# Optimization experiments

Hardware: AMD Instinct MI355X
Metric: run time of the kernel (lower is better)

## Reference

```python
import jax, jax.numpy as jnp
import numpy as np

B_, L_, D_, H_ = 2, 1024, 1024, 16


def _matrixR(L, d_model):
    # Transformer-XL sinusoid table, reversed along the position axis (reverse=True)
    inv_freq = 1.0 / (10000.0 ** (np.arange(0, d_model, 2, dtype=np.float32) / d_model))
    sinus = np.arange(L, dtype=np.float32)[:, None] * inv_freq[None, :]
    mat = np.zeros((L, d_model), dtype=np.float32)
    mat[:, 0::2] = np.sin(sinus)
    mat[:, 1::2] = np.cos(sinus)
    return jnp.asarray(mat[::-1].copy())


def _shift_b(x):
    # x: (b, h, L, L) -> TXL relative shift + lower-triangular mask
    b, h, L, _ = x.shape
    pad = jnp.concatenate([jnp.zeros((b, h, L, 1), x.dtype), x], axis=-1)  # (b,h,L,L+1)
    shifted = pad.reshape(b, h, L + 1, L)[:, :, 1:, :]                      # (b,h,L,L)
    return jnp.tril(shifted)


def setup_inputs() -> dict:
    key = jax.random.key(0)
    ks = jax.random.split(key, 8)
    s = 1.0 / np.sqrt(D_)
    return {
        "E": jax.random.normal(ks[0], (B_, L_, D_), dtype=jnp.float32),
        "Ev": jax.random.normal(ks[1], (B_, L_, D_), dtype=jnp.float32),
        "R": _matrixR(L_, D_),
        "Wq": jax.random.normal(ks[2], (D_, D_), dtype=jnp.float32) * s,
        "Wke": jax.random.normal(ks[3], (D_, D_), dtype=jnp.float32) * s,
        "Wkr": jax.random.normal(ks[4], (D_, D_), dtype=jnp.float32) * s,
        "Wv": jax.random.normal(ks[5], (D_, D_), dtype=jnp.float32) * s,
        "cb": jnp.ones((D_,), dtype=jnp.float32),
        "pb": jnp.ones((D_,), dtype=jnp.float32),
        "Wo_w": jax.random.normal(ks[6], (D_, D_), dtype=jnp.float32) * s,
        "Wo_b": jnp.zeros((D_,), dtype=jnp.float32),
        "ln_g": jnp.ones((D_,), dtype=jnp.float32),
        "ln_b": jnp.zeros((D_,), dtype=jnp.float32),
    }


def reference(E, Ev, R, Wq, Wke, Wkr, Wv, cb, pb, Wo_w, Wo_b, ln_g, ln_b):
    b, L, d = E.shape
    h = H_
    dh = d // h
    # projections -> (b, h, L, dh)
    q = (E @ Wq).reshape(b, L, h, dh).transpose(0, 2, 1, 3)
    k = (Ev @ Wke).reshape(b, L, h, dh).transpose(0, 2, 1, 3)
    v = (Ev @ Wv).reshape(b, L, h, dh).transpose(0, 2, 1, 3)
    # relative-position keys (batch independent): (h, L, dh)
    Q = (R @ Wkr).reshape(L, h, dh).transpose(1, 0, 2)
    # (a) content-content
    A_a = jnp.einsum('bhid,bhjd->bhij', q, k)
    # (b) content-position, with shift trick
    A_b = _shift_b(jnp.einsum('bhid,hjd->bhij', q, Q))
    # (c) global content bias (same for every query row)
    A_c = jnp.einsum('hd,bhjd->bhj', cb.reshape(h, dh), k)[:, :, None, :]  # (b,h,1,L)
    # (d) global position bias (batch independent), shifted
    d_row = jnp.einsum('hd,hjd->hj', pb.reshape(h, dh), Q)                 # (h,L)
    A_d = _shift_b(jnp.broadcast_to(d_row[None, :, None, :], (1, h, L, L)))
    A = A_a + A_b + A_c + A_d
    p = jax.nn.softmax(A, axis=-1)
    Oh = jnp.einsum('bhij,bhjd->bhid', p, v)
    O = Oh.transpose(0, 2, 1, 3).reshape(b, L, d)
    # residual + output proj (dropout is identity in eval) + LayerNorm
    res = Ev + (O @ Wo_w + Wo_b)
    mu = jnp.mean(res, axis=-1, keepdims=True)
    var = jnp.mean((res - mu) ** 2, axis=-1, keepdims=True)
    return (res - mu) * jax.lax.rsqrt(var + 1e-5) * ln_g + ln_b
```

## Files before the change

kernel.cpp:

```cpp
#include <hip/hip_runtime.h>
#include <hip/hip_bf16.h>
#include <math.h>

#define B_ 2
#define L_ 1024
#define D_ 1024
#define H_ 16

typedef short short8 __attribute__((ext_vector_type(8)));
typedef float f32x4  __attribute__((ext_vector_type(4)));

__device__ __forceinline__ short f2bf(float f) {
  unsigned u = __float_as_uint(f);
  u += 0x7fff + ((u >> 16) & 1);
  return (short)(u >> 16);
}
__device__ __forceinline__ float bf2f(short s) {
  return __uint_as_float(((unsigned)(unsigned short)s) << 16);
}
__device__ __forceinline__ int swz(int row, int slot) {
  return row * 64 + ((slot ^ (row & 7)) << 3);
}
__device__ __forceinline__ int vswz(int d, int j) {
  return d * 64 + ((((j >> 3) ^ (d & 7) ^ ((d >> 3) & 7)) & 7) << 3) + (j & 7);
}

__device__ __forceinline__ void glds16(const void* g, void* l) {
  __builtin_amdgcn_global_load_lds((const __attribute__((address_space(1))) void*)g,
                                   (__attribute__((address_space(3))) void*)l, 16, 0, 0);
}

__global__ __launch_bounds__(256) void castbf(
    const float* __restrict__ E, const float* __restrict__ Ev,
    const float* __restrict__ R, short* __restrict__ o) {
  size_t i8 = ((size_t)blockIdx.x * 256 + threadIdx.x) * 8;
  const float* src; size_t off;
  if (i8 < 2097152)      { src = E;  off = i8; }
  else if (i8 < 4194304) { src = Ev; off = i8 - 2097152; }
  else                   { src = R;  off = i8 - 4194304; }
  float4 a = *(const float4*)&src[off];
  float4 b = *(const float4*)&src[off + 4];
  short8 v;
  v[0] = f2bf(a.x); v[1] = f2bf(a.y); v[2] = f2bf(a.z); v[3] = f2bf(a.w);
  v[4] = f2bf(b.x); v[5] = f2bf(b.y); v[6] = f2bf(b.z); v[7] = f2bf(b.w);
  *(short8*)&o[i8] = v;
}

template<int OUT_F32>
__device__ __forceinline__ void mm_glds(const short* __restrict__ A,
                                        const short* __restrict__ Bt,
                                        void* Cp, int N, int K,
                                        int bx, int by) {
  __shared__ short As[8192];
  __shared__ short Bs[8192];
  const int tid = threadIdx.x;
  const int l = tid & 63, w = tid >> 6;
  const int row0 = by * 128, col0 = bx * 128;
  const int wm = (w >> 1) * 64, wn = (w & 1) * 64;
  const f32x4 fz = {0.f, 0.f, 0.f, 0.f};

  f32x4 acc[4][4];
  #pragma unroll
  for (int i = 0; i < 4; ++i)
    #pragma unroll
    for (int j = 0; j < 4; ++j) acc[i][j] = fz;

  const int lrow = l >> 3;
  const int lcol = (l & 7) * 8;

  for (int t = 0; t < K / 64; ++t) {
    const int k0 = t * 64;
    if (t) __syncthreads();
    #pragma unroll
    for (int c = 0; c < 4; ++c) {
      const int rr = (w * 4 + c) * 8 + lrow;
      glds16(&A[(size_t)(row0 + rr) * K + k0 + lcol], &As[(w * 4 + c) * 512]);
      glds16(&Bt[(size_t)(col0 + rr) * K + k0 + lcol], &Bs[(w * 4 + c) * 512]);
    }
    __syncthreads();
    #pragma unroll
    for (int kf = 0; kf < 2; ++kf) {
      short8 a[4], b[4];
      #pragma unroll
      for (int mf = 0; mf < 4; ++mf)
        a[mf] = *(const short8*)&As[(wm + mf * 16 + (l & 15)) * 64 + (kf * 4 + (l >> 4)) * 8];
      #pragma unroll
      for (int nf = 0; nf < 4; ++nf)
        b[nf] = *(const short8*)&Bs[(wn + nf * 16 + (l & 15)) * 64 + (kf * 4 + (l >> 4)) * 8];
      #pragma unroll
      for (int mf = 0; mf < 4; ++mf)
        #pragma unroll
        for (int nf = 0; nf < 4; ++nf)
          acc[mf][nf] = __builtin_amdgcn_mfma_f32_16x16x32_bf16(a[mf], b[nf], acc[mf][nf], 0, 0, 0);
    }
  }

  #pragma unroll
  for (int mf = 0; mf < 4; ++mf)
    #pragma unroll
    for (int nf = 0; nf < 4; ++nf)
      #pragma unroll
      for (int r = 0; r < 4; ++r) {
        int row = row0 + wm + mf * 16 + (l >> 4) * 4 + r;
        int col = col0 + wn + nf * 16 + (l & 15);
        if (OUT_F32) ((float*)Cp)[(size_t)row * N + col] = acc[mf][nf][r];
        else         ((short*)Cp)[(size_t)row * N + col] = f2bf(acc[mf][nf][r]);
      }
}

__global__ __launch_bounds__(256) void proj_mfma(
    const short* __restrict__ Eb, const short* __restrict__ Evb,
    const short* __restrict__ Rb, const short* __restrict__ Wt,
    short* __restrict__ qb, short* __restrict__ kb,
    short* __restrict__ vb, short* __restrict__ Qpb) {
  const int z = blockIdx.z;
  const short* A; const short* Bt; short* C; int M;
  const size_t MM = (size_t)D_ * D_;
  if (z == 0)      { A = Eb;  Bt = Wt;          C = qb;  M = B_ * L_; }
  else if (z == 1) { A = Evb; Bt = Wt + MM;     C = kb;  M = B_ * L_; }
  else if (z == 2) { A = Evb; Bt = Wt + 3 * MM; C = vb;  M = B_ * L_; }
  else             { A = Rb;  Bt = Wt + 2 * MM; C = Qpb; M = L_;      }
  if ((int)blockIdx.y * 128 >= M) return;
  mm_glds<0>(A, Bt, C, D_, D_, blockIdx.x, blockIdx.y);
}

__global__ __launch_bounds__(256) void out_mfma(
    const short* __restrict__ Ob, const short* __restrict__ Wot, float* __restrict__ proj) {
  mm_glds<1>(Ob, Wot, proj, D_, D_, blockIdx.x, blockIdx.y);
}

__global__ __launch_bounds__(256) void tcast(
    const float* __restrict__ W0, const float* __restrict__ W1,
    const float* __restrict__ W2, const float* __restrict__ W3,
    const float* __restrict__ W4, short* __restrict__ out) {
  const int z = blockIdx.z;
  const float* W = (z == 0) ? W0 : (z == 1) ? W1 : (z == 2) ? W2 : (z == 3) ? W3 : W4;
  short* Wt = out + (size_t)z * D_ * D_;
  __shared__ short t[64][65];
  const int tid = threadIdx.x;
  const int r0 = blockIdx.y * 64, c0 = blockIdx.x * 64;
  #pragma unroll
  for (int i = 0; i < 4; ++i) {
    int idx = tid + i * 256;
    int r = idx >> 4, c4 = (idx & 15) * 4;
    float4 v = *(const float4*)&W[(size_t)(r0 + r) * D_ + c0 + c4];
    t[c4 + 0][r] = f2bf(v.x); t[c4 + 1][r] = f2bf(v.y);
    t[c4 + 2][r] = f2bf(v.z); t[c4 + 3][r] = f2bf(v.w);
  }
  __syncthreads();
  #pragma unroll
  for (int i = 0; i < 2; ++i) {
    int idx = tid + i * 256;
    int rr = idx >> 3, cc = (idx & 7) * 8;
    short8 o;
    #pragma unroll
    for (int e = 0; e < 8; ++e) o[e] = t[rr][cc + e];
    *(short8*)&Wt[(size_t)(c0 + rr) * D_ + r0 + cc] = o;
  }
}

__global__ __launch_bounds__(256) void cdvec(
    const short* __restrict__ kb, const short* __restrict__ Qpb,
    const float* __restrict__ cb, const float* __restrict__ pb,
    float* __restrict__ cvec, float* __restrict__ dvec) {
  int idx = blockIdx.x * 256 + threadIdx.x;
  if (idx < B_ * H_ * L_) {
    int b = idx >> 14, h = (idx >> 10) & 15, j = idx & 1023;
    const short* kr = &kb[(size_t)(b * L_ + j) * D_ + h * 64];
    const float* cr = &cb[h * 64];
    float s = 0.f;
    #pragma unroll
    for (int d8 = 0; d8 < 8; ++d8) {
      short8 kv = *(const short8*)&kr[d8 * 8];
      #pragma unroll
      for (int e = 0; e < 8; ++e) s += bf2f(kv[e]) * cr[d8 * 8 + e];
    }
    cvec[idx] = s;
  } else {
    int i2 = idx - B_ * H_ * L_;
    if (i2 < H_ * L_) {
      int h = i2 >> 10, m = i2 & 1023;
      const short* qr = &Qpb[(size_t)m * D_ + h * 64];
      const float* pr = &pb[h * 64];
      float s = 0.f;
      #pragma unroll
      for (int d8 = 0; d8 < 8; ++d8) {
        short8 qv = *(const short8*)&qr[d8 * 8];
        #pragma unroll
        for (int e = 0; e < 8; ++e) s += bf2f(qv[e]) * pr[d8 * 8 + e];
      }
      dvec[i2] = s;
    }
  }
}

__global__ __launch_bounds__(256) void attn_mfma(
    const short* __restrict__ qb, const short* __restrict__ kb,
    const short* __restrict__ vb, const short* __restrict__ Qpb,
    const float* __restrict__ cvec, const float* __restrict__ dvec,
    short* __restrict__ Ob) {
  __shared__ short q_s[4096];
  __shared__ short k_s[4096];
  __shared__ short vt_s[4096];
  __shared__ short win_s[8192];
  __shared__ short pb_s[4 * 1312];
  __shared__ float cvec_s[64];
  __shared__ float dvec_s[128];

  const int tid = threadIdx.x;
  const int l = tid & 63, w = tid >> 6;
  const int nib = L_ / 64;
  const int b  = blockIdx.x / (H_ * nib);
  const int hh = (blockIdx.x / nib) % H_;
  const int i0 = (blockIdx.x % nib) * 64;
  const f32x4 fz = {0.f, 0.f, 0.f, 0.f};
  const short8 sz = {0, 0, 0, 0, 0, 0, 0, 0};

  short8 rk[2], rv[2], rw[4];
  float rc = 0.f, rd = 0.f;

  auto stage_load = [&](int jt) {
    const int j0 = jt * 64;
    const bool pos = (j0 <= i0);
    const int mbase = L_ - 64 - i0 + j0;
    #pragma unroll
    for (int c = 0; c < 2; ++c) {
      int ci = tid + c * 256;
      int r = ci >> 3, s = ci & 7;
      rk[c] = *(const short8*)&kb[(size_t)(b * L_ + j0 + r) * D_ + hh * 64 + s * 8];
      rv[c] = *(const short8*)&vb[(size_t)(b * L_ + j0 + r) * D_ + hh * 64 + s * 8];
    }
    if (pos) {
      #pragma unroll
      for (int c = 0; c < 4; ++c) {
        int ci = tid + c * 256;
        int mm = ci >> 3, s = ci & 7;
        int m = mbase + mm;
        rw[c] = (m < L_) ? *(const short8*)&Qpb[(size_t)m * D_ + hh * 64 + s * 8] : sz;
      }
      if (tid < 128) {
        int m = mbase + tid;
        rd = (m < L_) ? dvec[hh * L_ + m] : 0.f;
      }
    }
    if (tid < 64) rc = cvec[(size_t)(b * H_ + hh) * L_ + j0 + tid];
  };

  auto stage_write = [&](int jt) {
    const bool pos = (jt * 64 <= i0);
    #pragma unroll
    for (int c = 0; c < 2; ++c) {
      int ci = tid + c * 256;
      int r = ci >> 3, s = ci & 7;
      *(short8*)&k_s[swz(r, s)] = rk[c];
      #pragma unroll
      for (int e = 0; e < 8; ++e) {
        int d = s * 8 + e;
        vt_s[vswz(d, r)] = rv[c][e];
      }
    }
    if (pos) {
      #pragma unroll
      for (int c = 0; c < 4; ++c) {
        int ci = tid + c * 256;
        int mm = ci >> 3, s = ci & 7;
        *(short8*)&win_s[swz(mm, s)] = rw[c];
      }
      if (tid < 128) dvec_s[tid] = rd;
    }
    if (tid < 64) cvec_s[tid] = rc;
  };

  short8 rq[2];
  #pragma unroll
  for (int c = 0; c < 2; ++c) {
    int ci = tid + c * 256;
    int r = ci >> 3, s = ci & 7;
    rq[c] = *(const short8*)&qb[(size_t)(b * L_ + i0 + r) * D_ + hh * 64 + s * 8];
  }
  stage_load(0);
  #pragma unroll
  for (int c = 0; c < 2; ++c) {
    int ci = tid + c * 256;
    *(short8*)&q_s[swz(ci >> 3, ci & 7)] = rq[c];
  }
  __syncthreads();

  short8 aq[2];
  {
    int row = w * 16 + (l & 15);
    aq[0] = *(const short8*)&q_s[swz(row, (l >> 4))];
    aq[1] = *(const short8*)&q_s[swz(row, 4 + (l >> 4))];
  }

  float mrow[4], lrow[4];
  f32x4 oacc[4];
  #pragma unroll
  for (int r = 0; r < 4; ++r) { mrow[r] = -3.0e38f; lrow[r] = 0.f; }
  #pragma unroll
  for (int nf = 0; nf < 4; ++nf) oacc[nf] = fz;

  for (int jt = 0; jt < 16; ++jt) {
    const int j0 = jt * 64;
    const bool pos = (j0 <= i0);
    const bool diag = (j0 == i0);

    stage_write(jt);
    __syncthreads();
    if (jt < 15) stage_load(jt + 1);

    f32x4 sac[4];
    #pragma unroll
    for (int nf = 0; nf < 4; ++nf) sac[nf] = fz;
    #pragma unroll
    for (int kf = 0; kf < 2; ++kf) {
      #pragma unroll
      for (int nf = 0; nf < 4; ++nf) {
        short8 bk = *(const short8*)&k_s[swz(nf * 16 + (l & 15), kf * 4 + (l >> 4))];
        sac[nf] = __builtin_amdgcn_mfma_f32_16x16x32_bf16(aq[kf], bk, sac[nf], 0, 0, 0);
      }
    }

    if (pos) {
      f32x4 pacc[5];
      #pragma unroll
      for (int u = 0; u < 5; ++u) pacc[u] = fz;
      const int nf0 = 3 - w;
      #pragma unroll
      for (int kf = 0; kf < 2; ++kf) {
        #pragma unroll
        for (int u = 0; u < 5; ++u) {
          short8 bw = *(const short8*)&win_s[swz((nf0 + u) * 16 + (l & 15), kf * 4 + (l >> 4))];
          pacc[u] = __builtin_amdgcn_mfma_f32_16x16x32_bf16(aq[kf], bw, pacc[u], 0, 0, 0);
        }
      }
      const int pbb = w * 1312;
      #pragma unroll
      for (int u = 0; u < 5; ++u)
        #pragma unroll
        for (int r = 0; r < 4; ++r) {
          int row = (l >> 4) * 4 + r;
          pb_s[pbb + row * 82 + u * 16 + (l & 15)] = f2bf(pacc[u][r]);
        }
    }

    #pragma unroll
    for (int nf = 0; nf < 4; ++nf)
      #pragma unroll
      for (int r = 0; r < 4; ++r) {
        int rj = nf * 16 + (l & 15);
        float s = sac[nf][r] + cvec_s[rj];
        if (pos) {
          int ris = (l >> 4) * 4 + r;
          int rib = w * 16 + ris;
          if (!diag || rj <= rib) {
            s += bf2f(pb_s[w * 1312 + ris * 82 + (15 - ris + rj)]);
            s += dvec_s[63 - rib + rj];
          }
        }
        sac[nf][r] = s;
      }

    #pragma unroll
    for (int r = 0; r < 4; ++r) {
      float mx = fmaxf(fmaxf(sac[0][r], sac[1][r]), fmaxf(sac[2][r], sac[3][r]));
      #pragma unroll
      for (int off = 1; off < 16; off <<= 1)
        mx = fmaxf(mx, __shfl_xor(mx, off, 64));
      float mn = fmaxf(mrow[r], mx);
      float sc = __expf(mrow[r] - mn);
      mrow[r] = mn;
      float ls = 0.f;
      #pragma unroll
      for (int nf = 0; nf < 4; ++nf) {
        float p = __expf(sac[nf][r] - mn);
        sac[nf][r] = p;
        ls += p;
      }
      #pragma unroll
      for (int off = 1; off < 16; off <<= 1)
        ls += __shfl_xor(ls, off, 64);
      lrow[r] = lrow[r] * sc + ls;
      #pragma unroll
      for (int nf = 0; nf < 4; ++nf) oacc[nf][r] *= sc;
    }

    #pragma unroll
    for (int nf = 0; nf < 4; ++nf)
      #pragma unroll
      for (int r = 0; r < 4; ++r) {
        int row = (l >> 4) * 4 + r;
        int col = nf * 16 + (l & 15);
        pb_s[w * 1312 + row * 64 + (((col >> 3) ^ (row & 7)) << 3) + (col & 7)] = f2bf(sac[nf][r]);
      }

    #pragma unroll
    for (int kf = 0; kf < 2; ++kf) {
      int prow = l & 15;
      short8 ap = *(const short8*)&pb_s[w * 1312 + prow * 64 + (((kf * 4 + (l >> 4)) ^ (prow & 7)) << 3)];
      #pragma unroll
      for (int nf = 0; nf < 4; ++nf) {
        short8 bv = *(const short8*)&vt_s[vswz(nf * 16 + (l & 15), (kf * 4 + (l >> 4)) * 8)];
        oacc[nf] = __builtin_amdgcn_mfma_f32_16x16x32_bf16(ap, bv, oacc[nf], 0, 0, 0);
      }
    }
    __syncthreads();
  }

  #pragma unroll
  for (int r = 0; r < 4; ++r) {
    float inv = 1.f / lrow[r];
    #pragma unroll
    for (int nf = 0; nf < 4; ++nf) {
      int row = i0 + w * 16 + (l >> 4) * 4 + r;
      int col = hh * 64 + nf * 16 + (l & 15);
      Ob[(size_t)(b * L_ + row) * D_ + col] = f2bf(oacc[nf][r] * inv);
    }
  }
}

__global__ __launch_bounds__(256) void ln_kernel(
    const float* __restrict__ Ev, const float* __restrict__ proj,
    const float* __restrict__ Wo_b, const float* __restrict__ g,
    const float* __restrict__ beta, float* __restrict__ out) {
  const int row = blockIdx.x;
  __shared__ float red[8];
  const int tid = threadIdx.x;
  const int d = tid * 4;

  float4 e  = *(const float4*)&Ev[(size_t)row * D_ + d];
  float4 p  = *(const float4*)&proj[(size_t)row * D_ + d];
  float4 wb = *(const float4*)&Wo_b[d];
  float4 rr = { e.x + p.x + wb.x, e.y + p.y + wb.y,
                e.z + p.z + wb.z, e.w + p.w + wb.w };
  float sum = rr.x + rr.y + rr.z + rr.w;
  float sq  = rr.x * rr.x + rr.y * rr.y + rr.z * rr.z + rr.w * rr.w;

  #pragma unroll
  for (int off = 1; off < 64; off <<= 1) {
    sum += __shfl_xor(sum, off, 64);
    sq  += __shfl_xor(sq,  off, 64);
  }
  const int wid = tid >> 6;
  if ((tid & 63) == 0) { red[wid * 2] = sum; red[wid * 2 + 1] = sq; }
  __syncthreads();
  sum = red[0] + red[2] + red[4] + red[6];
  sq  = red[1] + red[3] + red[5] + red[7];

  const float mu   = sum * (1.f / (float)D_);
  const float var  = sq * (1.f / (float)D_) - mu * mu;
  const float rstd = rsqrtf(var + 1e-5f);

  float4 gg = *(const float4*)&g[d];
  float4 bb = *(const float4*)&beta[d];
  float4 o = { (rr.x - mu) * rstd * gg.x + bb.x,
               (rr.y - mu) * rstd * gg.y + bb.y,
               (rr.z - mu) * rstd * gg.z + bb.z,
               (rr.w - mu) * rstd * gg.w + bb.w };
  *(float4*)&out[(size_t)row * D_ + d] = o;
}

extern "C" void kernel_launch(void* const* d_in, const int* in_sizes, int n_in,
                              void* d_out, int out_size, void* d_ws, size_t ws_size,
                              hipStream_t stream) {
  const float* E    = (const float*)d_in[0];
  const float* Ev   = (const float*)d_in[1];
  const float* R    = (const float*)d_in[2];
  const float* Wq   = (const float*)d_in[3];
  const float* Wke  = (const float*)d_in[4];
  const float* Wkr  = (const float*)d_in[5];
  const float* Wv   = (const float*)d_in[6];
  const float* cb   = (const float*)d_in[7];
  const float* pb   = (const float*)d_in[8];
  const float* Wo_w = (const float*)d_in[9];
  const float* Wo_b = (const float*)d_in[10];
  const float* ln_g = (const float*)d_in[11];
  const float* ln_b = (const float*)d_in[12];
  float* out = (float*)d_out;

  short* ws   = (short*)d_ws;
  short* Eb   = ws;
  short* Evb  = ws + 2097152;
  short* Rb   = ws + 4194304;
  short* qb   = ws + 5242880;
  short* kb   = ws + 7340032;
  short* vb   = ws + 9437184;
  short* Qpb  = ws + 11534336;
  short* Wt   = ws + 12582912;
  short* Ob   = ws + 17825792;
  float* proj = (float*)Eb;
  float* cvec = (float*)Rb;
  float* dvec = cvec + 32768;

  castbf<<<2560, 256, 0, stream>>>(E, Ev, R, Eb);

  tcast<<<dim3(16, 16, 5), 256, 0, stream>>>(Wq, Wke, Wkr, Wv, Wo_w, Wt);

  proj_mfma<<<dim3(8, 16, 4), 256, 0, stream>>>(Eb, Evb, Rb, Wt, qb, kb, vb, Qpb);

  cdvec<<<192, 256, 0, stream>>>(kb, Qpb, cb, pb, cvec, dvec);

  attn_mfma<<<B_ * H_ * (L_ / 64), 256, 0, stream>>>(qb, kb, vb, Qpb, cvec, dvec, Ob);

  out_mfma<<<dim3(8, 16), 256, 0, stream>>>(Ob, Wt + 4 * (size_t)D_ * D_, proj);

  ln_kernel<<<B_ * L_, 256, 0, stream>>>(Ev, proj, Wo_b, ln_g, ln_b, out);
}
```

Baseline: 227.0 us.

## Rewrite pipeline with single-wave direct-load GEMMs, fused biases, transposed V

Replaces the LDS-tiled 128x128 GEMMs with single-wave 32x64 tiles that load operands straight from global memory, and merges the activation cast and weight transpose kernels into one launch. The cvec/dvec kernel is removed by folding the content and position biases into q before the score MFMAs. V is written transposed by the projection so the attention kernel can read it directly. Attention now runs one wave per 16-row tile with no shared-memory staging or block barriers, using setprio around the MFMA sections. This cuts kernel launches and synchronisation, but relies on cache hits instead of LDS reuse and issues more redundant global loads.

```diff
diff --git a/kernel.cpp b/kernel.cpp
--- a/kernel.cpp
+++ b/kernel.cpp
@@ -8,6 +8,7 @@
 #define H_ 16
 
 typedef short short8 __attribute__((ext_vector_type(8)));
+typedef short short4v __attribute__((ext_vector_type(4)));
 typedef float f32x4  __attribute__((ext_vector_type(4)));
 
 __device__ __forceinline__ short f2bf(float f) {
@@ -18,127 +19,40 @@
 __device__ __forceinline__ float bf2f(short s) {
   return __uint_as_float(((unsigned)(unsigned short)s) << 16);
 }
-__device__ __forceinline__ int swz(int row, int slot) {
-  return row * 64 + ((slot ^ (row & 7)) << 3);
-}
-__device__ __forceinline__ int vswz(int d, int j) {
-  return d * 64 + ((((j >> 3) ^ (d & 7) ^ ((d >> 3) & 7)) & 7) << 3) + (j & 7);
-}
-
-__device__ __forceinline__ void glds16(const void* g, void* l) {
-  __builtin_amdgcn_global_load_lds((const __attribute__((address_space(1))) void*)g,
-                                   (__attribute__((address_space(3))) void*)l, 16, 0, 0);
-}
-
-__global__ __launch_bounds__(256) void castbf(
+__device__ __forceinline__ int pkey(int row) {
+  return (row & 7) ^ ((row & 8) >> 2);
+}
+
+__global__ __launch_bounds__(256) void prep(
     const float* __restrict__ E, const float* __restrict__ Ev,
-    const float* __restrict__ R, short* __restrict__ o) {
-  size_t i8 = ((size_t)blockIdx.x * 256 + threadIdx.x) * 8;
-  const float* src; size_t off;
-  if (i8 < 2097152)      { src = E;  off = i8; }
-  else if (i8 < 4194304) { src = Ev; off = i8 - 2097152; }
-  else                   { src = R;  off = i8 - 4194304; }
-  float4 a = *(const float4*)&src[off];
-  float4 b = *(const float4*)&src[off + 4];
-  short8 v;
-  v[0] = f2bf(a.x); v[1] = f2bf(a.y); v[2] = f2bf(a.z); v[3] = f2bf(a.w);
-  v[4] = f2bf(b.x); v[5] = f2bf(b.y); v[6] = f2bf(b.z); v[7] = f2bf(b.w);
-  *(short8*)&o[i8] = v;
-}
-
-template<int OUT_F32>
-__device__ __forceinline__ void mm_glds(const short* __restrict__ A,
-                                        const short* __restrict__ Bt,
-                                        void* Cp, int N, int K,
-                                        int bx, int by) {
-  __shared__ short As[8192];
-  __shared__ short Bs[8192];
-  const int tid = threadIdx.x;
-  const int l = tid & 63, w = tid >> 6;
-  const int row0 = by * 128, col0 = bx * 128;
-  const int wm = (w >> 1) * 64, wn = (w & 1) * 64;
-  const f32x4 fz = {0.f, 0.f, 0.f, 0.f};
-
-  f32x4 acc[4][4];
-  #pragma unroll
-  for (int i = 0; i < 4; ++i)
-    #pragma unroll
-    for (int j = 0; j < 4; ++j) acc[i][j] = fz;
-
-  const int lrow = l >> 3;
-  const int lcol = (l & 7) * 8;
-
-  for (int t = 0; t < K / 64; ++t) {
-    const int k0 = t * 64;
-    if (t) __syncthreads();
-    #pragma unroll
-    for (int c = 0; c < 4; ++c) {
-      const int rr = (w * 4 + c) * 8 + lrow;
-      glds16(&A[(size_t)(row0 + rr) * K + k0 + lcol], &As[(w * 4 + c) * 512]);
-      glds16(&Bt[(size_t)(col0 + rr) * K + k0 + lcol], &Bs[(w * 4 + c) * 512]);
-    }
-    __syncthreads();
-    #pragma unroll
-    for (int kf = 0; kf < 2; ++kf) {
-      short8 a[4], b[4];
-      #pragma unroll
-      for (int mf = 0; mf < 4; ++mf)
-        a[mf] = *(const short8*)&As[(wm + mf * 16 + (l & 15)) * 64 + (kf * 4 + (l >> 4)) * 8];
-      #pragma unroll
-      for (int nf = 0; nf < 4; ++nf)
-        b[nf] = *(const short8*)&Bs[(wn + nf * 16 + (l & 15)) * 64 + (kf * 4 + (l >> 4)) * 8];
-      #pragma unroll
-      for (int mf = 0; mf < 4; ++mf)
-        #pragma unroll
-        for (int nf = 0; nf < 4; ++nf)
-          acc[mf][nf] = __builtin_amdgcn_mfma_f32_16x16x32_bf16(a[mf], b[nf], acc[mf][nf], 0, 0, 0);
-    }
-  }
-
-  #pragma unroll
-  for (int mf = 0; mf < 4; ++mf)
-    #pragma unroll
-    for (int nf = 0; nf < 4; ++nf)
-      #pragma unroll
-      for (int r = 0; r < 4; ++r) {
-        int row = row0 + wm + mf * 16 + (l >> 4) * 4 + r;
-        int col = col0 + wn + nf * 16 + (l & 15);
-        if (OUT_F32) ((float*)Cp)[(size_t)row * N + col] = acc[mf][nf][r];
-        else         ((short*)Cp)[(size_t)row * N + col] = f2bf(acc[mf][nf][r]);
-      }
-}
-
-__global__ __launch_bounds__(256) void proj_mfma(
-    const short* __restrict__ Eb, const short* __restrict__ Evb,
-    const short* __restrict__ Rb, const short* __restrict__ Wt,
-    short* __restrict__ qb, short* __restrict__ kb,
-    short* __restrict__ vb, short* __restrict__ Qpb) {
-  const int z = blockIdx.z;
-  const short* A; const short* Bt; short* C; int M;
-  const size_t MM = (size_t)D_ * D_;
-  if (z == 0)      { A = Eb;  Bt = Wt;          C = qb;  M = B_ * L_; }
-  else if (z == 1) { A = Evb; Bt = Wt + MM;     C = kb;  M = B_ * L_; }
-  else if (z == 2) { A = Evb; Bt = Wt + 3 * MM; C = vb;  M = B_ * L_; }
-  else             { A = Rb;  Bt = Wt + 2 * MM; C = Qpb; M = L_;      }
-  if ((int)blockIdx.y * 128 >= M) return;
-  mm_glds<0>(A, Bt, C, D_, D_, blockIdx.x, blockIdx.y);
-}
-
-__global__ __launch_bounds__(256) void out_mfma(
-    const short* __restrict__ Ob, const short* __restrict__ Wot, float* __restrict__ proj) {
-  mm_glds<1>(Ob, Wot, proj, D_, D_, blockIdx.x, blockIdx.y);
-}
-
-__global__ __launch_bounds__(256) void tcast(
+    const float* __restrict__ R,
     const float* __restrict__ W0, const float* __restrict__ W1,
     const float* __restrict__ W2, const float* __restrict__ W3,
-    const float* __restrict__ W4, short* __restrict__ out) {
-  const int z = blockIdx.z;
-  const float* W = (z == 0) ? W0 : (z == 1) ? W1 : (z == 2) ? W2 : (z == 3) ? W3 : W4;
-  short* Wt = out + (size_t)z * D_ * D_;
+    const float* __restrict__ W4,
+    short* __restrict__ act, short* __restrict__ Wt) {
   __shared__ short t[64][65];
   const int tid = threadIdx.x;
-  const int r0 = blockIdx.y * 64, c0 = blockIdx.x * 64;
+  int bid = blockIdx.x;
+  if (bid < 2560) {
+    size_t i8 = ((size_t)bid * 256 + tid) * 8;
+    const float* src; size_t off;
+    if (i8 < 2097152)      { src = E;  off = i8; }
+    else if (i8 < 4194304) { src = Ev; off = i8 - 2097152; }
+    else                   { src = R;  off = i8 - 4194304; }
+    float4 a = *(const float4*)&src[off];
+    float4 b = *(const float4*)&src[off + 4];
+    short8 v;
+    v[0] = f2bf(a.x); v[1] = f2bf(a.y); v[2] = f2bf(a.z); v[3] = f2bf(a.w);
+    v[4] = f2bf(b.x); v[5] = f2bf(b.y); v[6] = f2bf(b.z); v[7] = f2bf(b.w);
+    *(short8*)&act[i8] = v;
+    return;
+  }
+  bid -= 2560;
+  const int z = bid >> 8, rem = bid & 255;
+  const int by = rem >> 4, bx = rem & 15;
+  const float* W = (z == 0) ? W0 : (z == 1) ? W1 : (z == 2) ? W2 : (z == 3) ? W3 : W4;
+  short* Wtz = Wt + (size_t)z * D_ * D_;
+  const int r0 = by * 64, c0 = bx * 64;
   #pragma unroll
   for (int i = 0; i < 4; ++i) {
     int idx = tid + i * 256;
@@ -155,143 +69,133 @@
     short8 o;
     #pragma unroll
     for (int e = 0; e < 8; ++e) o[e] = t[rr][cc + e];
-    *(short8*)&Wt[(size_t)(c0 + rr) * D_ + r0 + cc] = o;
-  }
-}
-
-__global__ __launch_bounds__(256) void cdvec(
-    const short* __restrict__ kb, const short* __restrict__ Qpb,
+    *(short8*)&Wtz[(size_t)(c0 + rr) * D_ + r0 + cc] = o;
+  }
+}
+
+template<int OUT>
+__device__ __forceinline__ void mmd(const short* __restrict__ A,
+                                    const short* __restrict__ Bt,
+                                    void* __restrict__ Cp,
+                                    int bx, int by) {
+  const int l = threadIdx.x & 63;
+  const int row0 = by * 32, col0 = bx * 64;
+  const f32x4 fz = {0.f, 0.f, 0.f, 0.f};
+
+  f32x4 acc[2][4];
+  #pragma unroll
+  for (int i = 0; i < 2; ++i)
+    #pragma unroll
+    for (int j = 0; j < 4; ++j) acc[i][j] = fz;
+
+  const short* Ap = &A[(size_t)(row0 + (l & 15)) * 1024 + (l >> 4) * 8];
+  const short* Bp = &Bt[(size_t)(col0 + (l & 15)) * 1024 + (l >> 4) * 8];
+
+  #pragma unroll 2
+  for (int kk = 0; kk < 32; ++kk) {
+    const int ko = kk * 32;
+    short8 a0 = *(const short8*)(Ap + ko);
+    short8 a1 = *(const short8*)(Ap + 16384 + ko);
+    short8 b0 = *(const short8*)(Bp + ko);
+    short8 b1 = *(const short8*)(Bp + 16384 + ko);
+    short8 b2 = *(const short8*)(Bp + 32768 + ko);
+    short8 b3 = *(const short8*)(Bp + 49152 + ko);
+    acc[0][0] = __builtin_amdgcn_mfma_f32_16x16x32_bf16(a0, b0, acc[0][0], 0, 0, 0);
+    acc[0][1] = __builtin_amdgcn_mfma_f32_16x16x32_bf16(a0, b1, acc[0][1], 0, 0, 0);
+    acc[0][2] = __builtin_amdgcn_mfma_f32_16x16x32_bf16(a0, b2, acc[0][2], 0, 0, 0);
+    acc[0][3] = __builtin_amdgcn_mfma_f32_16x16x32_bf16(a0, b3, acc[0][3], 0, 0, 0);
+    acc[1][0] = __builtin_amdgcn_mfma_f32_16x16x32_bf16(a1, b0, acc[1][0], 0, 0, 0);
+    acc[1][1] = __builtin_amdgcn_mfma_f32_16x16x32_bf16(a1, b1, acc[1][1], 0, 0, 0);
+    acc[1][2] = __builtin_amdgcn_mfma_f32_16x16x32_bf16(a1, b2, acc[1][2], 0, 0, 0);
+    acc[1][3] = __builtin_amdgcn_mfma_f32_16x16x32_bf16(a1, b3, acc[1][3], 0, 0, 0);
+  }
+
+  #pragma unroll
+  for (int mf = 0; mf < 2; ++mf)
+    #pragma unroll
+    for (int nf = 0; nf < 4; ++nf) {
+      if (OUT == 2) {
+        int tok = row0 + mf * 16 + (l >> 4) * 4;
+        int col = col0 + nf * 16 + (l & 15);
+        int bb = tok >> 10, j = tok & 1023;
+        int h = col >> 6, d = col & 63;
+        short4v o;
+        #pragma unroll
+        for (int r = 0; r < 4; ++r) o[r] = f2bf(acc[mf][nf][r]);
+        *(short4v*)&((short*)Cp)[((size_t)((bb * H_ + h) * 64 + d)) * 1024 + j] = o;
+      } else {
+        #pragma unroll
+        for (int r = 0; r < 4; ++r) {
+          int row = row0 + mf * 16 + (l >> 4) * 4 + r;
+          int col = col0 + nf * 16 + (l & 15);
+          if (OUT == 1) ((float*)Cp)[(size_t)row * 1024 + col] = acc[mf][nf][r];
+          else          ((short*)Cp)[(size_t)row * 1024 + col] = f2bf(acc[mf][nf][r]);
+        }
+      }
+    }
+}
+
+__global__ __launch_bounds__(64) void proj_g(
+    const short* __restrict__ Eb, const short* __restrict__ Evb,
+    const short* __restrict__ Rb, const short* __restrict__ Wt,
+    short* __restrict__ qb, short* __restrict__ kb,
+    short* __restrict__ vt, short* __restrict__ Qpb) {
+  const int z = blockIdx.z;
+  const int bx = blockIdx.x & 15, by = blockIdx.x >> 4;
+  const size_t MM = (size_t)D_ * D_;
+  const short* A; const short* Bt; short* C; int M;
+  if (z == 0)      { A = Eb;  Bt = Wt;          C = qb;  M = B_ * L_; }
+  else if (z == 1) { A = Evb; Bt = Wt + MM;     C = kb;  M = B_ * L_; }
+  else if (z == 2) { A = Evb; Bt = Wt + 3 * MM; C = vt;  M = B_ * L_; }
+  else             { A = Rb;  Bt = Wt + 2 * MM; C = Qpb; M = L_;      }
+  if (by * 32 >= M) return;
+  if (z == 2) mmd<2>(A, Bt, C, bx, by);
+  else        mmd<0>(A, Bt, C, bx, by);
+}
+
+__global__ __launch_bounds__(64) void out_g(
+    const short* __restrict__ Ob, const short* __restrict__ Wot,
+    float* __restrict__ proj) {
+  mmd<1>(Ob, Wot, proj, blockIdx.x & 15, blockIdx.x >> 4);
+}
+
+__global__ __launch_bounds__(64) void attn_d(
+    const short* __restrict__ qb, const short* __restrict__ kb,
+    const short* __restrict__ vt, const short* __restrict__ Qpb,
     const float* __restrict__ cb, const float* __restrict__ pb,
-    float* __restrict__ cvec, float* __restrict__ dvec) {
-  int idx = blockIdx.x * 256 + threadIdx.x;
-  if (idx < B_ * H_ * L_) {
-    int b = idx >> 14, h = (idx >> 10) & 15, j = idx & 1023;
-    const short* kr = &kb[(size_t)(b * L_ + j) * D_ + h * 64];
-    const float* cr = &cb[h * 64];
-    float s = 0.f;
-    #pragma unroll
-    for (int d8 = 0; d8 < 8; ++d8) {
-      short8 kv = *(const short8*)&kr[d8 * 8];
-      #pragma unroll
-      for (int e = 0; e < 8; ++e) s += bf2f(kv[e]) * cr[d8 * 8 + e];
-    }
-    cvec[idx] = s;
-  } else {
-    int i2 = idx - B_ * H_ * L_;
-    if (i2 < H_ * L_) {
-      int h = i2 >> 10, m = i2 & 1023;
-      const short* qr = &Qpb[(size_t)m * D_ + h * 64];
-      const float* pr = &pb[h * 64];
-      float s = 0.f;
-      #pragma unroll
-      for (int d8 = 0; d8 < 8; ++d8) {
-        short8 qv = *(const short8*)&qr[d8 * 8];
-        #pragma unroll
-        for (int e = 0; e < 8; ++e) s += bf2f(qv[e]) * pr[d8 * 8 + e];
-      }
-      dvec[i2] = s;
-    }
-  }
-}
-
-__global__ __launch_bounds__(256) void attn_mfma(
-    const short* __restrict__ qb, const short* __restrict__ kb,
-    const short* __restrict__ vb, const short* __restrict__ Qpb,
-    const float* __restrict__ cvec, const float* __restrict__ dvec,
     short* __restrict__ Ob) {
-  __shared__ short q_s[4096];
-  __shared__ short k_s[4096];
-  __shared__ short vt_s[4096];
-  __shared__ short win_s[8192];
-  __shared__ short pb_s[4 * 1312];
-  __shared__ float cvec_s[64];
-  __shared__ float dvec_s[128];
-
-  const int tid = threadIdx.x;
-  const int l = tid & 63, w = tid >> 6;
-  const int nib = L_ / 64;
-  const int b  = blockIdx.x / (H_ * nib);
-  const int hh = (blockIdx.x / nib) % H_;
-  const int i0 = (blockIdx.x % nib) * 64;
+  __shared__ short pbs[1312];
+
+  const int l = threadIdx.x & 63;
+  const int hl = blockIdx.x & 31;
+  const int it = blockIdx.x >> 5;
+  const int b = hl >> 4, hh = hl & 15;
+  const int i0 = it * 16;
   const f32x4 fz = {0.f, 0.f, 0.f, 0.f};
-  const short8 sz = {0, 0, 0, 0, 0, 0, 0, 0};
-
-  short8 rk[2], rv[2], rw[4];
-  float rc = 0.f, rd = 0.f;
-
-  auto stage_load = [&](int jt) {
-    const int j0 = jt * 64;
-    const bool pos = (j0 <= i0);
-    const int mbase = L_ - 64 - i0 + j0;
-    #pragma unroll
-    for (int c = 0; c < 2; ++c) {
-      int ci = tid + c * 256;
-      int r = ci >> 3, s = ci & 7;
-      rk[c] = *(const short8*)&kb[(size_t)(b * L_ + j0 + r) * D_ + hh * 64 + s * 8];
-      rv[c] = *(const short8*)&vb[(size_t)(b * L_ + j0 + r) * D_ + hh * 64 + s * 8];
-    }
-    if (pos) {
-      #pragma unroll
-      for (int c = 0; c < 4; ++c) {
-        int ci = tid + c * 256;
-        int mm = ci >> 3, s = ci & 7;
-        int m = mbase + mm;
-        rw[c] = (m < L_) ? *(const short8*)&Qpb[(size_t)m * D_ + hh * 64 + s * 8] : sz;
-      }
-      if (tid < 128) {
-        int m = mbase + tid;
-        rd = (m < L_) ? dvec[hh * L_ + m] : 0.f;
-      }
-    }
-    if (tid < 64) rc = cvec[(size_t)(b * H_ + hh) * L_ + j0 + tid];
-  };
-
-  auto stage_write = [&](int jt) {
-    const bool pos = (jt * 64 <= i0);
-    #pragma unroll
-    for (int c = 0; c < 2; ++c) {
-      int ci = tid + c * 256;
-      int r = ci >> 3, s = ci & 7;
-      *(short8*)&k_s[swz(r, s)] = rk[c];
+
+  short8 aqc[2], aqp[2];
+  {
+    const size_t qoff = (size_t)(b * L_ + i0 + (l & 15)) * D_ + hh * 64 + (l >> 4) * 8;
+    #pragma unroll
+    for (int kf = 0; kf < 2; ++kf) {
+      short8 qv = *(const short8*)&qb[qoff + kf * 32];
+      f32x4 c0 = *(const f32x4*)&cb[hh * 64 + kf * 32 + (l >> 4) * 8];
+      f32x4 c1 = *(const f32x4*)&cb[hh * 64 + kf * 32 + (l >> 4) * 8 + 4];
+      f32x4 p0 = *(const f32x4*)&pb[hh * 64 + kf * 32 + (l >> 4) * 8];
+      f32x4 p1 = *(const f32x4*)&pb[hh * 64 + kf * 32 + (l >> 4) * 8 + 4];
       #pragma unroll
       for (int e = 0; e < 8; ++e) {
-        int d = s * 8 + e;
-        vt_s[vswz(d, r)] = rv[c][e];
-      }
-    }
-    if (pos) {
-      #pragma unroll
-      for (int c = 0; c < 4; ++c) {
-        int ci = tid + c * 256;
-        int mm = ci >> 3, s = ci & 7;
-        *(short8*)&win_s[swz(mm, s)] = rw[c];
-      }
-      if (tid < 128) dvec_s[tid] = rd;
-    }
-    if (tid < 64) cvec_s[tid] = rc;
-  };
-
-  short8 rq[2];
-  #pragma unroll
-  for (int c = 0; c < 2; ++c) {
-    int ci = tid + c * 256;
-    int r = ci >> 3, s = ci & 7;
-    rq[c] = *(const short8*)&qb[(size_t)(b * L_ + i0 + r) * D_ + hh * 64 + s * 8];
-  }
-  stage_load(0);
-  #pragma unroll
-  for (int c = 0; c < 2; ++c) {
-    int ci = tid + c * 256;
-    *(short8*)&q_s[swz(ci >> 3, ci & 7)] = rq[c];
-  }
-  __syncthreads();
-
-  short8 aq[2];
-  {
-    int row = w * 16 + (l & 15);
-    aq[0] = *(const short8*)&q_s[swz(row, (l >> 4))];
-    aq[1] = *(const short8*)&q_s[swz(row, 4 + (l >> 4))];
-  }
+        float q = bf2f(qv[e]);
+        float cc = (e < 4) ? c0[e] : c1[e - 4];
+        float pp = (e < 4) ? p0[e] : p1[e - 4];
+        aqc[kf][e] = f2bf(q + cc);
+        aqp[kf][e] = f2bf(q + pp);
+      }
+    }
+  }
+
+  const short* kbase  = &kb[(size_t)(b * L_) * D_ + hh * 64 + (l >> 4) * 8];
+  const short* vtbase = &vt[(size_t)((b * H_ + hh) * 64) * 1024 + (l >> 4) * 8];
 
   float mrow[4], lrow[4];
   f32x4 oacc[4];
@@ -302,64 +206,57 @@
 
   for (int jt = 0; jt < 16; ++jt) {
     const int j0 = jt * 64;
-    const bool pos = (j0 <= i0);
-    const bool diag = (j0 == i0);
-
-    stage_write(jt);
-    __syncthreads();
-    if (jt < 15) stage_load(jt + 1);
+    const int dth = i0 - j0;
+    const bool pos = (dth >= -15);
+    const int mb = L_ - 16 - dth;
 
     f32x4 sac[4];
     #pragma unroll
     for (int nf = 0; nf < 4; ++nf) sac[nf] = fz;
+    __builtin_amdgcn_s_setprio(1);
     #pragma unroll
     for (int kf = 0; kf < 2; ++kf) {
       #pragma unroll
       for (int nf = 0; nf < 4; ++nf) {
-        short8 bk = *(const short8*)&k_s[swz(nf * 16 + (l & 15), kf * 4 + (l >> 4))];
-        sac[nf] = __builtin_amdgcn_mfma_f32_16x16x32_bf16(aq[kf], bk, sac[nf], 0, 0, 0);
-      }
-    }
+        short8 bk = *(const short8*)&kbase[(size_t)(j0 + nf * 16 + (l & 15)) * D_ + kf * 32];
+        sac[nf] = __builtin_amdgcn_mfma_f32_16x16x32_bf16(aqc[kf], bk, sac[nf], 0, 0, 0);
+      }
+    }
+    __builtin_amdgcn_s_setprio(0);
 
     if (pos) {
       f32x4 pacc[5];
       #pragma unroll
       for (int u = 0; u < 5; ++u) pacc[u] = fz;
-      const int nf0 = 3 - w;
+      __builtin_amdgcn_s_setprio(1);
       #pragma unroll
       for (int kf = 0; kf < 2; ++kf) {
         #pragma unroll
         for (int u = 0; u < 5; ++u) {
-          short8 bw = *(const short8*)&win_s[swz((nf0 + u) * 16 + (l & 15), kf * 4 + (l >> 4))];
-          pacc[u] = __builtin_amdgcn_mfma_f32_16x16x32_bf16(aq[kf], bw, pacc[u], 0, 0, 0);
+          int m = mb + u * 16 + (l & 15);
+          m = (m < L_) ? m : (L_ - 1);
+          short8 bw = *(const short8*)&Qpb[(size_t)m * D_ + hh * 64 + kf * 32 + (l >> 4) * 8];
+          pacc[u] = __builtin_amdgcn_mfma_f32_16x16x32_bf16(aqp[kf], bw, pacc[u], 0, 0, 0);
         }
       }
-      const int pbb = w * 1312;
+      __builtin_amdgcn_s_setprio(0);
       #pragma unroll
       for (int u = 0; u < 5; ++u)
         #pragma unroll
         for (int r = 0; r < 4; ++r) {
           int row = (l >> 4) * 4 + r;
-          pb_s[pbb + row * 82 + u * 16 + (l & 15)] = f2bf(pacc[u][r]);
+          pbs[row * 82 + u * 16 + (l & 15)] = f2bf(pacc[u][r]);
         }
-    }
-
-    #pragma unroll
-    for (int nf = 0; nf < 4; ++nf)
-      #pragma unroll
-      for (int r = 0; r < 4; ++r) {
-        int rj = nf * 16 + (l & 15);
-        float s = sac[nf][r] + cvec_s[rj];
-        if (pos) {
+      #pragma unroll
+      for (int nf = 0; nf < 4; ++nf)
+        #pragma unroll
+        for (int r = 0; r < 4; ++r) {
           int ris = (l >> 4) * 4 + r;
-          int rib = w * 16 + ris;
-          if (!diag || rj <= rib) {
-            s += bf2f(pb_s[w * 1312 + ris * 82 + (15 - ris + rj)]);
-            s += dvec_s[63 - rib + rj];
-          }
+          int rj = nf * 16 + (l & 15);
+          if (rj <= ris + dth)
+            sac[nf][r] += bf2f(pbs[ris * 82 + (15 - ris + rj)]);
         }
-        sac[nf][r] = s;
-      }
+    }
 
     #pragma unroll
     for (int r = 0; r < 4; ++r) {
@@ -391,20 +288,21 @@
       for (int r = 0; r < 4; ++r) {
         int row = (l >> 4) * 4 + r;
         int col = nf * 16 + (l & 15);
-        pb_s[w * 1312 + row * 64 + (((col >> 3) ^ (row & 7)) << 3) + (col & 7)] = f2bf(sac[nf][r]);
-      }
-
+        pbs[row * 64 + (((col >> 3) ^ pkey(row)) << 3) + (col & 7)] = f2bf(sac[nf][r]);
+      }
+
+    __builtin_amdgcn_s_setprio(1);
     #pragma unroll
     for (int kf = 0; kf < 2; ++kf) {
       int prow = l & 15;
-      short8 ap = *(const short8*)&pb_s[w * 1312 + prow * 64 + (((kf * 4 + (l >> 4)) ^ (prow & 7)) << 3)];
+      short8 ap = *(const short8*)&pbs[prow * 64 + (((kf * 4 + (l >> 4)) ^ pkey(prow)) << 3)];
       #pragma unroll
       for (int nf = 0; nf < 4; ++nf) {
-        short8 bv = *(const short8*)&vt_s[vswz(nf * 16 + (l & 15), (kf * 4 + (l >> 4)) * 8)];
+        short8 bv = *(const short8*)&vtbase[(size_t)(nf * 16 + (l & 15)) * 1024 + j0 + kf * 32];
         oacc[nf] = __builtin_amdgcn_mfma_f32_16x16x32_bf16(ap, bv, oacc[nf], 0, 0, 0);
       }
     }
-    __syncthreads();
+    __builtin_amdgcn_s_setprio(0);
   }
 
   #pragma unroll
@@ -412,7 +310,7 @@
     float inv = 1.f / lrow[r];
     #pragma unroll
     for (int nf = 0; nf < 4; ++nf) {
-      int row = i0 + w * 16 + (l >> 4) * 4 + r;
+      int row = i0 + (l >> 4) * 4 + r;
       int col = hh * 64 + nf * 16 + (l & 15);
       Ob[(size_t)(b * L_ + row) * D_ + col] = f2bf(oacc[nf][r] * inv);
     }
@@ -484,25 +382,19 @@
   short* Rb   = ws + 4194304;
   short* qb   = ws + 5242880;
   short* kb   = ws + 7340032;
-  short* vb   = ws + 9437184;
+  short* vt   = ws + 9437184;
   short* Qpb  = ws + 11534336;
   short* Wt   = ws + 12582912;
   short* Ob   = ws + 17825792;
   float* proj = (float*)Eb;
-  float* cvec = (float*)Rb;
-  float* dvec = cvec + 32768;
-
-  castbf<<<2560, 256, 0, stream>>>(E, Ev, R, Eb);
-
-  tcast<<<dim3(16, 16, 5), 256, 0, stream>>>(Wq, Wke, Wkr, Wv, Wo_w, Wt);
-
-  proj_mfma<<<dim3(8, 16, 4), 256, 0, stream>>>(Eb, Evb, Rb, Wt, qb, kb, vb, Qpb);
-
-  cdvec<<<192, 256, 0, stream>>>(kb, Qpb, cb, pb, cvec, dvec);
-
-  attn_mfma<<<B_ * H_ * (L_ / 64), 256, 0, stream>>>(qb, kb, vb, Qpb, cvec, dvec, Ob);
-
-  out_mfma<<<dim3(8, 16), 256, 0, stream>>>(Ob, Wt + 4 * (size_t)D_ * D_, proj);
+
+  prep<<<3840, 256, 0, stream>>>(E, Ev, R, Wq, Wke, Wkr, Wv, Wo_w, Eb, Wt);
+
+  proj_g<<<dim3(1024, 1, 4), 64, 0, stream>>>(Eb, Evb, Rb, Wt, qb, kb, vt, Qpb);
+
+  attn_d<<<2048, 64, 0, stream>>>(qb, kb, vt, Qpb, cb, pb, Ob);
+
+  out_g<<<1024, 64, 0, stream>>>(Ob, Wt + 4 * (size_t)D_ * D_, proj);
 
   ln_kernel<<<B_ * L_, 256, 0, stream>>>(Ev, proj, Wo_b, ln_g, ln_b, out);
 }
```

Result: slower. 299.9 us (+32.1%).
